# Kernel tuning notes

Measured on AMD Instinct MI355X. Metric: run time of the kernel, lower is better.

The kernel has to match this reference:

```python
import jax, jax.numpy as jnp
import numpy as np
from jax import lax

SCORE_THRESHOLD = 0.001
IOU_THRESHOLD = 0.7
MAX_DETECTIONS = 300
PRE_NMS_TOPK = 1024      # standard pre-NMS candidate cap (torchvision/YOLO practice)
CLASS_OFFSET = 4096.0    # > max image coord, separates classes so cross-class IoU == 0
IMG = 640.0

B, N, C = 32, 8400, 80


def setup_inputs() -> dict:
    key = jax.random.key(0)
    kc, ks, kp = jax.random.split(key, 3)
    # well-formed boxes in [y1, x1, y2, x2] convention (matches repo's nms())
    tl = jax.random.uniform(kc, (B, N, 2), jnp.float32, 0.0, IMG - 1.0)   # (y1, x1)
    wh = jax.random.uniform(ks, (B, N, 2), jnp.float32, 4.0, 160.0)      # (h, w)
    boxes = jnp.concatenate([tl, jnp.minimum(tl + wh, IMG)], axis=-1)     # [B,N,4]
    scores = jax.random.uniform(kp, (B, N, C), jnp.float32)               # [B,N,C]
    return {"boxes": boxes, "scores": scores}


def _pairwise_iou(b):
    # b: [B,K,4] as [y1,x1,y2,x2]; +1 pixel convention per the repo's nms()
    y1, x1, y2, x2 = b[..., 0], b[..., 1], b[..., 2], b[..., 3]
    areas = (x2 - x1 + 1.0) * (y2 - y1 + 1.0)                             # [B,K]
    yy1 = jnp.maximum(y1[:, :, None], y1[:, None, :])
    xx1 = jnp.maximum(x1[:, :, None], x1[:, None, :])
    yy2 = jnp.minimum(y2[:, :, None], y2[:, None, :])
    xx2 = jnp.minimum(x2[:, :, None], x2[:, None, :])
    w = jnp.maximum(0.0, xx2 - xx1 + 1.0)
    h = jnp.maximum(0.0, yy2 - yy1 + 1.0)
    inter = w * h                                                          # [B,K,K]
    return inter / (areas[:, :, None] + areas[:, None, :] - inter)


def multiclass_nms(boxes, scores):
    b, n, c = scores.shape
    flat = jnp.where(scores > SCORE_THRESHOLD, scores, 0.0).reshape(b, n * c)
    top_scores, top_idx = lax.top_k(flat, PRE_NMS_TOPK)                    # [B,K]
    box_idx = top_idx // c
    cls_idx = top_idx % c                                                  # int32 [B,K]
    cand = jnp.take_along_axis(boxes, box_idx[..., None], axis=1)          # [B,K,4]
    # offset boxes by class so per-class NMS happens in one shared pass
    off = cand + (cls_idx.astype(cand.dtype) * CLASS_OFFSET)[..., None]
    iou = _pairwise_iou(off)                                               # [B,K,K]

    k = PRE_NMS_TOPK
    idx = jnp.arange(k)
    keep0 = top_scores > SCORE_THRESHOLD                                   # [B,K]

    def body(i, keep):
        row = iou[:, i, :]                                                 # [B,K]
        sup = (row > IOU_THRESHOLD) & keep[:, i][:, None] & (idx[None, :] > i)
        return keep & ~sup

    keep = lax.fori_loop(0, k, body, keep0)                                # greedy NMS

    final_scores = jnp.where(keep, top_scores, 0.0)
    out_scores, sel = lax.top_k(final_scores, MAX_DETECTIONS)              # [B,300]
    out_boxes = jnp.take_along_axis(cand, sel[..., None], axis=1)          # [B,300,4]
    out_labels = jnp.take_along_axis(cls_idx, sel, axis=1)                 # [B,300]
    n_valid = jnp.minimum(jnp.sum(keep, axis=1, keepdims=True), MAX_DETECTIONS)
    return out_boxes, out_scores, out_labels.astype(jnp.int32), n_valid.astype(jnp.int32)


def reference(boxes, scores):
    return multiclass_nms(boxes, scores)
```

## Files before the change

### kernel.cpp

```cpp
#include <hip/hip_runtime.h>
#include <cstdint>
#include <cstddef>

#define B_      32
#define N_      8400
#define C_      80
#define NC      672000
#define NCV4    168000
#define NBINS   4096
#define TOPK    1024
#define MAXDET  300
#define CANDCAP 4096
#define NSLICE  16
#define SLICE_V4 10500
#define NBKT    8
#define SEGB    64
#define BSORT   256

#define STAGE_THRESH 0.998046875f

#define WS_SEGKEYS  0
#define WS_SEGCNT   2097152
#define WS_TOPSCORE 2113536
#define WS_TOPBOX   2244608
#define WS_TOPCLS   2768896
#define WS_KEEP     2899968

#define OUT_SCORES  38400
#define OUT_LABELS  48000
#define OUT_NVALID  57600

__global__ __launch_bounds__(256) void stage_kernel(const float4* __restrict__ scores4,
                                                    unsigned* __restrict__ segCnt,
                                                    unsigned long long* __restrict__ segKeys) {
    __shared__ unsigned lcnt[NBKT];
    int b = blockIdx.x, sl = blockIdx.y, tid = threadIdx.x;
    if (tid < NBKT) lcnt[tid] = 0;
    __syncthreads();
    const float4* s = scores4 + (size_t)b * NCV4 + (size_t)sl * SLICE_V4;
    for (int i = tid; i < SLICE_V4; i += 256) {
        float4 v = s[i];
        float c[4] = {v.x, v.y, v.z, v.w};
        unsigned flat0 = ((unsigned)sl * SLICE_V4 + (unsigned)i) * 4u;
        #pragma unroll
        for (int kc = 0; kc < 4; ++kc) {
            float x = (c[kc] > 0.001f) ? c[kc] : 0.0f;
            if (x >= STAGE_THRESH) {
                int bin = (int)(x * 4096.0f);
                bin = bin > (NBINS - 1) ? (NBINS - 1) : bin;
                int bkt = bin - 4088;
                unsigned p = atomicAdd(&lcnt[bkt], 1u);
                if (p < (unsigned)SEGB)
                    segKeys[(((size_t)(b * NBKT + bkt)) * NSLICE + sl) * SEGB + p] =
                        ((unsigned long long)__float_as_uint(x) << 32) |
                        (unsigned long long)(0xFFFFFFFFu - (flat0 + kc));
            }
        }
    }
    __syncthreads();
    if (tid < NBKT) segCnt[(b * NBKT + tid) * NSLICE + sl] = lcnt[tid];
}

__global__ __launch_bounds__(64) void sortb_kernel(
        const float4* __restrict__ scores4,
        const unsigned long long* __restrict__ segKeys,
        const unsigned* __restrict__ segCnt,
        const float4* __restrict__ boxes4,
        float* __restrict__ topScore,
        float4* __restrict__ topBox4,
        int* __restrict__ topCls) {
    __shared__ unsigned long long kbuf[CANDCAP];
    __shared__ unsigned bsum[NBKT];
    __shared__ unsigned bok[NBKT];
    __shared__ unsigned spref[NSLICE + 1];
    __shared__ unsigned scnt;
    __shared__ int s_cut;
    int b = blockIdx.x, bkt = blockIdx.y, lane = threadIdx.x;

    if (lane < NBKT) {
        const unsigned* c = segCnt + (b * NBKT + lane) * NSLICE;
        unsigned ssum = 0, ok = 1;
        for (int sl = 0; sl < NSLICE; ++sl) {
            unsigned v = c[sl];
            if (v > (unsigned)SEGB) ok = 0;
            ssum += v;
        }
        bsum[lane] = ssum; bok[lane] = ok;
    }
    __threadfence_block();
    unsigned M = 0, base = 0; int valid = 1;
    #pragma unroll
    for (int t = 0; t < NBKT; ++t) {
        unsigned s2 = bsum[t];
        if (!bok[t] || s2 > (unsigned)BSORT) valid = 0;
        M += s2;
        if (t > bkt) base += s2;
    }
    unsigned n = bsum[bkt];
    if (M < (unsigned)TOPK || M > (unsigned)CANDCAP) valid = 0;

    if (valid) {
        if (base >= (unsigned)TOPK || n == 0) return;
        if (lane == 0) {
            unsigned acc = 0; spref[0] = 0;
            const unsigned* c = segCnt + (b * NBKT + bkt) * NSLICE;
            for (int sl = 0; sl < NSLICE; ++sl) { acc += c[sl]; spref[sl + 1] = acc; }
        }
        __threadfence_block();
        for (int sl = 0; sl < NSLICE; ++sl) {
            unsigned b0 = spref[sl], c2 = spref[sl + 1] - b0;
            const unsigned long long* src =
                segKeys + (((size_t)(b * NBKT + bkt)) * NSLICE + sl) * SEGB;
            for (unsigned t = lane; t < c2; t += 64) kbuf[b0 + t] = src[t];
        }
        for (unsigned t = n + lane; t < (unsigned)BSORT; t += 64) kbuf[t] = 0ull;
        __threadfence_block();
        for (int kk = 2; kk <= BSORT; kk <<= 1) {
            for (int j = kk >> 1; j > 0; j >>= 1) {
                for (int c2 = lane; c2 < BSORT / 2; c2 += 64) {
                    int t = ((c2 & ~(j - 1)) << 1) | (c2 & (j - 1));
                    int l = t | j;
                    unsigned long long a0 = kbuf[t], c0 = kbuf[l];
                    bool sw = ((t & kk) == 0) ? (a0 < c0) : (a0 > c0);
                    if (sw) { kbuf[t] = c0; kbuf[l] = a0; }
                }
                __threadfence_block();
            }
        }
        unsigned wlim = (unsigned)TOPK - base; if (wlim > n) wlim = n;
        for (unsigned r = lane; r < wlim; r += 64) {
            unsigned long long key = kbuf[r];
            float sc = __uint_as_float((unsigned)(key >> 32));
            unsigned idx = 0xFFFFFFFFu - (unsigned)(key & 0xFFFFFFFFull);
            if (idx >= (unsigned)NC) idx = 0;
            unsigned bi = idx / (unsigned)C_;
            unsigned cl = idx - bi * (unsigned)C_;
            unsigned pos = base + r;
            topScore[b * TOPK + pos] = sc;
            topBox4[b * TOPK + pos] = boxes4[(size_t)b * N_ + bi];
            topCls[b * TOPK + pos] = (int)cl;
        }
        return;
    }

    if (bkt != 0) return;
    unsigned* fh = (unsigned*)kbuf;
    for (int i2 = lane; i2 < NBINS; i2 += 64) fh[i2] = 0;
    if (lane == 0) scnt = 0;
    __threadfence_block();
    const float4* s = scores4 + (size_t)b * NCV4;
    for (int i2 = lane; i2 < NCV4; i2 += 64) {
        float4 v = s[i2];
        float c4[4] = {v.x, v.y, v.z, v.w};
        #pragma unroll
        for (int kc = 0; kc < 4; ++kc) {
            float x = (c4[kc] > 0.001f) ? c4[kc] : 0.0f;
            int bin = (int)(x * 4096.0f);
            bin = bin > (NBINS - 1) ? (NBINS - 1) : bin;
            atomicAdd(&fh[bin], 1u);
        }
    }
    __threadfence_block();
    if (lane == 0) {
        unsigned acc = 0; int cb = 0;
        for (int bin = NBINS - 1; bin >= 0; --bin) {
            acc += fh[bin];
            if (acc >= (unsigned)TOPK) { cb = bin; break; }
        }
        s_cut = cb;
    }
    __threadfence_block();
    int cb = s_cut;
    for (int i2 = lane; i2 < NCV4; i2 += 64) {
        float4 v = s[i2];
        float c4[4] = {v.x, v.y, v.z, v.w};
        unsigned flat0 = (unsigned)i2 * 4u;
        #pragma unroll
        for (int kc = 0; kc < 4; ++kc) {
            float x = (c4[kc] > 0.001f) ? c4[kc] : 0.0f;
            int bin = (int)(x * 4096.0f);
            bin = bin > (NBINS - 1) ? (NBINS - 1) : bin;
            if (bin >= cb) {
                unsigned p = atomicAdd(&scnt, 1u);
                if (p < (unsigned)CANDCAP)
                    kbuf[p] = ((unsigned long long)__float_as_uint(x) << 32) |
                              (unsigned long long)(0xFFFFFFFFu - (flat0 + kc));
            }
        }
    }
    __threadfence_block();
    unsigned M2 = scnt; if (M2 > (unsigned)CANDCAP) M2 = CANDCAP;
    int S = (M2 <= 1024u) ? 1024 : (M2 <= 2048u ? 2048 : CANDCAP);
    for (int i2 = (int)M2 + lane; i2 < S; i2 += 64) kbuf[i2] = 0ull;
    __threadfence_block();
    for (int kk = 2; kk <= S; kk <<= 1) {
        for (int j = kk >> 1; j > 0; j >>= 1) {
            for (int t = lane; t < S; t += 64) {
                int l = t ^ j;
                if (l > t) {
                    unsigned long long a0 = kbuf[t], c0 = kbuf[l];
                    bool sw = ((t & kk) == 0) ? (a0 < c0) : (a0 > c0);
                    if (sw) { kbuf[t] = c0; kbuf[l] = a0; }
                }
            }
            __threadfence_block();
        }
    }
    for (int r = lane; r < TOPK; r += 64) {
        unsigned long long key = kbuf[r];
        float sc = __uint_as_float((unsigned)(key >> 32));
        unsigned idx = 0xFFFFFFFFu - (unsigned)(key & 0xFFFFFFFFull);
        if (idx >= (unsigned)NC) idx = 0;
        unsigned bi = idx / (unsigned)C_;
        unsigned cl = idx - bi * (unsigned)C_;
        topScore[b * TOPK + r] = sc;
        topBox4[b * TOPK + r] = boxes4[(size_t)b * N_ + bi];
        topCls[b * TOPK + r] = (int)cl;
    }
}

#define CLS_CAP 256
__global__ __launch_bounds__(64) void nms_kernel(const float* __restrict__ topScore,
                                                 const float* __restrict__ topBox,
                                                 const int* __restrict__ topCls,
                                                 int* __restrict__ keep) {
    __shared__ unsigned short pos[CLS_CAP];
    __shared__ float by1[CLS_CAP], bx1[CLS_CAP], by2[CLS_CAP], bx2[CLS_CAP];
    __shared__ float barea[CLS_CAP];
    __shared__ unsigned char sup[CLS_CAP];
    int b = blockIdx.x;
    int c = blockIdx.y;
    int lane = threadIdx.x;
    const float* ts = topScore + b * TOPK;
    const int*   tc = topCls + b * TOPK;
    int*         kp = keep + b * TOPK;
    float off = (float)c * 4096.0f;
    int base = 0;
    for (int chunkS = 0; chunkS < TOPK; chunkS += 64) {
        int i = chunkS + lane;
        int cls = tc[i];
        float sc = ts[i];
        bool mine = (cls == c);
        bool listed = mine && (sc > 0.001f);
        if (mine) kp[i] = 0;
        unsigned long long mask = __ballot(listed);
        int rank = __popcll(mask & ((1ull << lane) - 1ull));
        if (listed) {
            int slot = base + rank;
            if (slot < CLS_CAP) {
                pos[slot] = (unsigned short)i;
                const float* tb = topBox + ((size_t)(b * TOPK + i)) * 4;
                float y1 = tb[0] + off, x1 = tb[1] + off;
                float y2 = tb[2] + off, x2 = tb[3] + off;
                by1[slot] = y1; bx1[slot] = x1; by2[slot] = y2; bx2[slot] = x2;
                barea[slot] = __fmul_rn((x2 - x1) + 1.0f, (y2 - y1) + 1.0f);
                sup[slot] = 0;
            }
        }
        base += __popcll(mask);
    }
    int m = base < CLS_CAP ? base : CLS_CAP;
    __syncthreads();
    int cur = 0;
    while (cur < m) {
        if (lane == 0) kp[pos[cur]] = 1;
        float cy1 = by1[cur], cx1 = bx1[cur], cy2 = by2[cur], cx2 = bx2[cur];
        float carea = barea[cur];
        for (int j = cur + 1 + lane; j < m; j += 64) {
            if (!sup[j]) {
                float yy1 = fmaxf(cy1, by1[j]), xx1 = fmaxf(cx1, bx1[j]);
                float yy2 = fminf(cy2, by2[j]), xx2 = fminf(cx2, bx2[j]);
                float w = fmaxf(0.0f, (xx2 - xx1) + 1.0f);
                float h = fmaxf(0.0f, (yy2 - yy1) + 1.0f);
                float inter = __fmul_rn(w, h);
                float denom = (carea + barea[j]) - inter;
                float iou = inter / denom;
                if (iou > 0.7f) sup[j] = 1;
            }
        }
        __syncthreads();
        int nxt = m;
        for (int j = cur + 1 + lane; j < m; j += 64)
            if (!sup[j]) { nxt = j; break; }
        for (int o = 32; o > 0; o >>= 1) {
            int other = __shfl_xor(nxt, o, 64);
            nxt = nxt < other ? nxt : other;
        }
        cur = nxt;
    }
}

__global__ __launch_bounds__(1024) void finalize_kernel(const float* __restrict__ topScore,
                                                        const float* __restrict__ topBox,
                                                        const int* __restrict__ topCls,
                                                        const int* __restrict__ keep,
                                                        float* __restrict__ out) {
    __shared__ int sk[TOPK];
    __shared__ int sel[MAXDET];
    int b = blockIdx.x;
    int i = threadIdx.x;
    int kp = keep[b * TOPK + i];
    sk[i] = kp;
    __syncthreads();
    for (int off = 1; off < TOPK; off <<= 1) {
        int add = (i >= off) ? sk[i - off] : 0;
        __syncthreads();
        sk[i] += add;
        __syncthreads();
    }
    int nk = sk[TOPK - 1];
    int incl = sk[i];
    int kexcl = incl - kp;
    int sexcl = i - kexcl;
    if (kp) {
        if (kexcl < MAXDET) sel[kexcl] = i;
    } else {
        int slot = nk + sexcl;
        if (slot < MAXDET) sel[slot] = i;
    }
    __syncthreads();
    if (i < MAXDET) {
        int p = sel[i];
        float sc = (i < nk) ? topScore[b * TOPK + p] : 0.0f;
        const float* tb = topBox + ((size_t)b * TOPK + p) * 4;
        float* ob = out + ((size_t)b * MAXDET + i) * 4;
        ob[0] = tb[0]; ob[1] = tb[1]; ob[2] = tb[2]; ob[3] = tb[3];
        out[OUT_SCORES + b * MAXDET + i] = sc;
        out[OUT_LABELS + b * MAXDET + i] = (float)topCls[b * TOPK + p];
    }
    if (i == 0) out[OUT_NVALID + b] = (float)(nk < MAXDET ? nk : MAXDET);
}

extern "C" void kernel_launch(void* const* d_in, const int* in_sizes, int n_in,
                              void* d_out, int out_size, void* d_ws, size_t ws_size,
                              hipStream_t stream) {
    const float* boxes  = (const float*)d_in[0];
    const float* scores = (const float*)d_in[1];
    float* out = (float*)d_out;
    char* ws = (char*)d_ws;

    unsigned long long* segKeys = (unsigned long long*)(ws + WS_SEGKEYS);
    unsigned* segCnt = (unsigned*)(ws + WS_SEGCNT);
    float* topScore = (float*)(ws + WS_TOPSCORE);
    float* topBox = (float*)(ws + WS_TOPBOX);
    int* topCls = (int*)(ws + WS_TOPCLS);
    int* keep = (int*)(ws + WS_KEEP);

    const float4* scores4 = (const float4*)scores;
    const float4* boxes4  = (const float4*)boxes;

    stage_kernel<<<dim3(B_, NSLICE), 256, 0, stream>>>(scores4, segCnt, segKeys);
    sortb_kernel<<<dim3(B_, NBKT), 64, 0, stream>>>(scores4, segKeys, segCnt, boxes4,
                                                    topScore, (float4*)topBox, topCls);
    nms_kernel<<<dim3(B_, C_), 64, 0, stream>>>(topScore, topBox, topCls, keep);
    finalize_kernel<<<B_, 1024, 0, stream>>>(topScore, topBox, topCls, keep, out);
}
```

Before: 190.0 us.

## Fuse sort, per-class NMS and finalize into one per-image block kernel

Replaces the sort, NMS and finalize kernels with a single 1024-thread block per image that keeps top-K scores, classes, boxes and keep flags in shared memory. The bitonic sort of each bucket becomes a rank-by-counting sort, and per-class NMS runs as 16 waves each handling several classes with the per-class cap lowered to 128. This removes two kernel launches and the global-memory round trips for intermediates. In exchange each image now runs on only 32 blocks, so NMS parallelism across classes drops from 80 blocks per image to 16 waves, and the fallback path runs within one block per image.

New measurement: 223.5 us. 1.18x slower.

```diff
diff --git a/kernel.cpp b/kernel.cpp
--- a/kernel.cpp
+++ b/kernel.cpp
@@ -16,15 +16,12 @@
 #define NBKT    8
 #define SEGB    64
 #define BSORT   256
+#define CLS_CAP 128
 
 #define STAGE_THRESH 0.998046875f
 
 #define WS_SEGKEYS  0
 #define WS_SEGCNT   2097152
-#define WS_TOPSCORE 2113536
-#define WS_TOPBOX   2244608
-#define WS_TOPCLS   2768896
-#define WS_KEEP     2899968
 
 #define OUT_SCORES  38400
 #define OUT_LABELS  48000
@@ -61,274 +58,287 @@
     if (tid < NBKT) segCnt[(b * NBKT + tid) * NSLICE + sl] = lcnt[tid];
 }
 
-__global__ __launch_bounds__(64) void sortb_kernel(
+__global__ __launch_bounds__(1024) void fused_kernel(
         const float4* __restrict__ scores4,
         const unsigned long long* __restrict__ segKeys,
         const unsigned* __restrict__ segCnt,
         const float4* __restrict__ boxes4,
-        float* __restrict__ topScore,
-        float4* __restrict__ topBox4,
-        int* __restrict__ topCls) {
-    __shared__ unsigned long long kbuf[CANDCAP];
+        float* __restrict__ out) {
+    __shared__ unsigned scnt2[NBKT][NSLICE];
     __shared__ unsigned bsum[NBKT];
     __shared__ unsigned bok[NBKT];
-    __shared__ unsigned spref[NSLICE + 1];
-    __shared__ unsigned scnt;
-    __shared__ int s_cut;
-    int b = blockIdx.x, bkt = blockIdx.y, lane = threadIdx.x;
-
-    if (lane < NBKT) {
-        const unsigned* c = segCnt + (b * NBKT + lane) * NSLICE;
+    __shared__ unsigned spref[NBKT][NSLICE];
+    __shared__ float   sScore[TOPK];
+    __shared__ int     sCls[TOPK];
+    __shared__ int     sBoxIdx[TOPK];
+    __shared__ float4  sBox[TOPK];
+    __shared__ int     sKeep[TOPK];
+    __shared__ int     sk[TOPK];
+    __shared__ int     sel[MAXDET];
+    __shared__ int     s_cut;
+    __shared__ unsigned s_scnt;
+    __shared__ __align__(16) char upool[49152];
+    unsigned long long* kbuf = (unsigned long long*)upool;
+    unsigned* fh = (unsigned*)(upool + 32768);
+    float* ny1 = (float*)upool;
+    float* nx1 = ny1 + 16 * CLS_CAP;
+    float* ny2 = nx1 + 16 * CLS_CAP;
+    float* nx2 = ny2 + 16 * CLS_CAP;
+    float* nar = nx2 + 16 * CLS_CAP;
+    unsigned short* npos = (unsigned short*)(nar + 16 * CLS_CAP);
+    unsigned char*  nsup = (unsigned char*)(npos + 16 * CLS_CAP);
+
+    int b = blockIdx.x;
+    int tid = threadIdx.x;
+    int lane = tid & 63;
+    int wave = tid >> 6;
+
+    if (tid < NBKT * NSLICE)
+        scnt2[tid >> 4][tid & 15] = segCnt[b * NBKT * NSLICE + tid];
+    __syncthreads();
+    if (tid < NBKT) {
         unsigned ssum = 0, ok = 1;
+        #pragma unroll
         for (int sl = 0; sl < NSLICE; ++sl) {
-            unsigned v = c[sl];
+            unsigned v = scnt2[tid][sl];
             if (v > (unsigned)SEGB) ok = 0;
             ssum += v;
         }
-        bsum[lane] = ssum; bok[lane] = ok;
-    }
-    __threadfence_block();
-    unsigned M = 0, base = 0; int valid = 1;
+        bsum[tid] = ssum; bok[tid] = ok;
+    }
+    if (tid < NBKT * NSLICE) {
+        int bkt = tid >> 4, sl = tid & 15;
+        unsigned acc = 0;
+        for (int s2 = 0; s2 < sl; ++s2) acc += scnt2[bkt][s2];
+        spref[bkt][sl] = acc;
+    }
+    __syncthreads();
+    unsigned M = 0; int valid = 1;
     #pragma unroll
     for (int t = 0; t < NBKT; ++t) {
         unsigned s2 = bsum[t];
         if (!bok[t] || s2 > (unsigned)BSORT) valid = 0;
         M += s2;
-        if (t > bkt) base += s2;
-    }
-    unsigned n = bsum[bkt];
+    }
     if (M < (unsigned)TOPK || M > (unsigned)CANDCAP) valid = 0;
 
     if (valid) {
-        if (base >= (unsigned)TOPK || n == 0) return;
-        if (lane == 0) {
-            unsigned acc = 0; spref[0] = 0;
-            const unsigned* c = segCnt + (b * NBKT + bkt) * NSLICE;
-            for (int sl = 0; sl < NSLICE; ++sl) { acc += c[sl]; spref[sl + 1] = acc; }
-        }
-        __threadfence_block();
-        for (int sl = 0; sl < NSLICE; ++sl) {
-            unsigned b0 = spref[sl], c2 = spref[sl + 1] - b0;
+        for (int seg = wave; seg < NBKT * NSLICE; seg += 16) {
+            int bkt = seg >> 4, sl = seg & 15;
+            unsigned c2 = scnt2[bkt][sl];
             const unsigned long long* src =
                 segKeys + (((size_t)(b * NBKT + bkt)) * NSLICE + sl) * SEGB;
-            for (unsigned t = lane; t < c2; t += 64) kbuf[b0 + t] = src[t];
-        }
-        for (unsigned t = n + lane; t < (unsigned)BSORT; t += 64) kbuf[t] = 0ull;
-        __threadfence_block();
-        for (int kk = 2; kk <= BSORT; kk <<= 1) {
+            if ((unsigned)lane < c2)
+                kbuf[bkt * BSORT + spref[bkt][sl] + lane] = src[lane];
+        }
+        __syncthreads();
+        int bkt = tid >> 7;
+        unsigned n = bsum[bkt];
+        unsigned base = 0;
+        for (int t = bkt + 1; t < NBKT; ++t) base += bsum[t];
+        if (base < (unsigned)TOPK && n > 0) {
+            const unsigned long long* kb = kbuf + bkt * BSORT;
+            int j0 = tid & 127, j1 = j0 + 128;
+            unsigned long long k0 = (j0 < (int)n) ? kb[j0] : 0ull;
+            unsigned long long k1 = (j1 < (int)n) ? kb[j1] : 0ull;
+            unsigned r0 = 0, r1 = 0;
+            for (unsigned i = 0; i < n; ++i) {
+                unsigned long long ki = kb[i];
+                r0 += (ki > k0); r1 += (ki > k1);
+            }
+            if (j0 < (int)n) {
+                unsigned pos = base + r0;
+                if (pos < (unsigned)TOPK) {
+                    unsigned idx = 0xFFFFFFFFu - (unsigned)(k0 & 0xFFFFFFFFull);
+                    if (idx >= (unsigned)NC) idx = 0;
+                    unsigned bi = idx / (unsigned)C_;
+                    sScore[pos] = __uint_as_float((unsigned)(k0 >> 32));
+                    sCls[pos] = (int)(idx - bi * (unsigned)C_);
+                    sBoxIdx[pos] = (int)bi;
+                }
+            }
+            if (j1 < (int)n) {
+                unsigned pos = base + r1;
+                if (pos < (unsigned)TOPK) {
+                    unsigned idx = 0xFFFFFFFFu - (unsigned)(k1 & 0xFFFFFFFFull);
+                    if (idx >= (unsigned)NC) idx = 0;
+                    unsigned bi = idx / (unsigned)C_;
+                    sScore[pos] = __uint_as_float((unsigned)(k1 >> 32));
+                    sCls[pos] = (int)(idx - bi * (unsigned)C_);
+                    sBoxIdx[pos] = (int)bi;
+                }
+            }
+        }
+    } else {
+        for (int i = tid; i < NBINS; i += 1024) fh[i] = 0;
+        if (tid == 0) s_scnt = 0;
+        __syncthreads();
+        const float4* s = scores4 + (size_t)b * NCV4;
+        for (int i = tid; i < NCV4; i += 1024) {
+            float4 v = s[i];
+            float c4[4] = {v.x, v.y, v.z, v.w};
+            #pragma unroll
+            for (int kc = 0; kc < 4; ++kc) {
+                float x = (c4[kc] > 0.001f) ? c4[kc] : 0.0f;
+                int bin = (int)(x * 4096.0f);
+                bin = bin > (NBINS - 1) ? (NBINS - 1) : bin;
+                atomicAdd(&fh[bin], 1u);
+            }
+        }
+        __syncthreads();
+        if (tid == 0) {
+            unsigned acc = 0; int cb2 = 0;
+            for (int bin = NBINS - 1; bin >= 0; --bin) {
+                acc += fh[bin];
+                if (acc >= (unsigned)TOPK) { cb2 = bin; break; }
+            }
+            s_cut = cb2;
+        }
+        __syncthreads();
+        int cb = s_cut;
+        for (int i = tid; i < NCV4; i += 1024) {
+            float4 v = s[i];
+            float c4[4] = {v.x, v.y, v.z, v.w};
+            unsigned flat0 = (unsigned)i * 4u;
+            #pragma unroll
+            for (int kc = 0; kc < 4; ++kc) {
+                float x = (c4[kc] > 0.001f) ? c4[kc] : 0.0f;
+                int bin = (int)(x * 4096.0f);
+                bin = bin > (NBINS - 1) ? (NBINS - 1) : bin;
+                if (bin >= cb) {
+                    unsigned p = atomicAdd(&s_scnt, 1u);
+                    if (p < (unsigned)CANDCAP)
+                        kbuf[p] = ((unsigned long long)__float_as_uint(x) << 32) |
+                                  (unsigned long long)(0xFFFFFFFFu - (flat0 + kc));
+                }
+            }
+        }
+        __syncthreads();
+        unsigned M2 = s_scnt; if (M2 > (unsigned)CANDCAP) M2 = CANDCAP;
+        int S = (M2 <= 1024u) ? 1024 : (M2 <= 2048u ? 2048 : CANDCAP);
+        for (int i = (int)M2 + tid; i < S; i += 1024) kbuf[i] = 0ull;
+        __syncthreads();
+        for (int kk = 2; kk <= S; kk <<= 1) {
             for (int j = kk >> 1; j > 0; j >>= 1) {
-                for (int c2 = lane; c2 < BSORT / 2; c2 += 64) {
-                    int t = ((c2 & ~(j - 1)) << 1) | (c2 & (j - 1));
-                    int l = t | j;
-                    unsigned long long a0 = kbuf[t], c0 = kbuf[l];
-                    bool sw = ((t & kk) == 0) ? (a0 < c0) : (a0 > c0);
-                    if (sw) { kbuf[t] = c0; kbuf[l] = a0; }
-                }
-                __threadfence_block();
-            }
-        }
-        unsigned wlim = (unsigned)TOPK - base; if (wlim > n) wlim = n;
-        for (unsigned r = lane; r < wlim; r += 64) {
+                for (int t = tid; t < S; t += 1024) {
+                    int l = t ^ j;
+                    if (l > t) {
+                        unsigned long long a0 = kbuf[t], c0 = kbuf[l];
+                        bool sw = ((t & kk) == 0) ? (a0 < c0) : (a0 > c0);
+                        if (sw) { kbuf[t] = c0; kbuf[l] = a0; }
+                    }
+                }
+                __syncthreads();
+            }
+        }
+        for (int r = tid; r < TOPK; r += 1024) {
             unsigned long long key = kbuf[r];
-            float sc = __uint_as_float((unsigned)(key >> 32));
             unsigned idx = 0xFFFFFFFFu - (unsigned)(key & 0xFFFFFFFFull);
             if (idx >= (unsigned)NC) idx = 0;
             unsigned bi = idx / (unsigned)C_;
-            unsigned cl = idx - bi * (unsigned)C_;
-            unsigned pos = base + r;
-            topScore[b * TOPK + pos] = sc;
-            topBox4[b * TOPK + pos] = boxes4[(size_t)b * N_ + bi];
-            topCls[b * TOPK + pos] = (int)cl;
-        }
-        return;
-    }
-
-    if (bkt != 0) return;
-    unsigned* fh = (unsigned*)kbuf;
-    for (int i2 = lane; i2 < NBINS; i2 += 64) fh[i2] = 0;
-    if (lane == 0) scnt = 0;
-    __threadfence_block();
-    const float4* s = scores4 + (size_t)b * NCV4;
-    for (int i2 = lane; i2 < NCV4; i2 += 64) {
-        float4 v = s[i2];
-        float c4[4] = {v.x, v.y, v.z, v.w};
-        #pragma unroll
-        for (int kc = 0; kc < 4; ++kc) {
-            float x = (c4[kc] > 0.001f) ? c4[kc] : 0.0f;
-            int bin = (int)(x * 4096.0f);
-            bin = bin > (NBINS - 1) ? (NBINS - 1) : bin;
-            atomicAdd(&fh[bin], 1u);
-        }
-    }
-    __threadfence_block();
-    if (lane == 0) {
-        unsigned acc = 0; int cb = 0;
-        for (int bin = NBINS - 1; bin >= 0; --bin) {
-            acc += fh[bin];
-            if (acc >= (unsigned)TOPK) { cb = bin; break; }
-        }
-        s_cut = cb;
-    }
-    __threadfence_block();
-    int cb = s_cut;
-    for (int i2 = lane; i2 < NCV4; i2 += 64) {
-        float4 v = s[i2];
-        float c4[4] = {v.x, v.y, v.z, v.w};
-        unsigned flat0 = (unsigned)i2 * 4u;
-        #pragma unroll
-        for (int kc = 0; kc < 4; ++kc) {
-            float x = (c4[kc] > 0.001f) ? c4[kc] : 0.0f;
-            int bin = (int)(x * 4096.0f);
-            bin = bin > (NBINS - 1) ? (NBINS - 1) : bin;
-            if (bin >= cb) {
-                unsigned p = atomicAdd(&scnt, 1u);
-                if (p < (unsigned)CANDCAP)
-                    kbuf[p] = ((unsigned long long)__float_as_uint(x) << 32) |
-                              (unsigned long long)(0xFFFFFFFFu - (flat0 + kc));
-            }
-        }
-    }
-    __threadfence_block();
-    unsigned M2 = scnt; if (M2 > (unsigned)CANDCAP) M2 = CANDCAP;
-    int S = (M2 <= 1024u) ? 1024 : (M2 <= 2048u ? 2048 : CANDCAP);
-    for (int i2 = (int)M2 + lane; i2 < S; i2 += 64) kbuf[i2] = 0ull;
-    __threadfence_block();
-    for (int kk = 2; kk <= S; kk <<= 1) {
-        for (int j = kk >> 1; j > 0; j >>= 1) {
-            for (int t = lane; t < S; t += 64) {
-                int l = t ^ j;
-                if (l > t) {
-                    unsigned long long a0 = kbuf[t], c0 = kbuf[l];
-                    bool sw = ((t & kk) == 0) ? (a0 < c0) : (a0 > c0);
-                    if (sw) { kbuf[t] = c0; kbuf[l] = a0; }
+            sScore[r] = __uint_as_float((unsigned)(key >> 32));
+            sCls[r] = (int)(idx - bi * (unsigned)C_);
+            sBoxIdx[r] = (int)bi;
+        }
+    }
+    __syncthreads();
+
+    {
+        int bi = sBoxIdx[tid];
+        sKeep[tid] = 0;
+        sBox[tid] = boxes4[(size_t)b * N_ + bi];
+    }
+    __syncthreads();
+
+    for (int c = wave; c < C_; c += 16) {
+        float off = (float)c * 4096.0f;
+        int base2 = 0;
+        for (int chunkS = 0; chunkS < TOPK; chunkS += 64) {
+            int i = chunkS + lane;
+            int cls = sCls[i];
+            float sc = sScore[i];
+            bool listed = (cls == c) && (sc > 0.001f);
+            unsigned long long mask = __ballot(listed);
+            int rank = __popcll(mask & ((1ull << lane) - 1ull));
+            if (listed) {
+                int slot = base2 + rank;
+                if (slot < CLS_CAP) {
+                    int s5 = wave * CLS_CAP + slot;
+                    float4 tb = sBox[i];
+                    float y1 = tb.x + off, x1 = tb.y + off;
+                    float y2 = tb.z + off, x2 = tb.w + off;
+                    npos[s5] = (unsigned short)i;
+                    ny1[s5] = y1; nx1[s5] = x1; ny2[s5] = y2; nx2[s5] = x2;
+                    nar[s5] = __fmul_rn((x2 - x1) + 1.0f, (y2 - y1) + 1.0f);
+                    nsup[s5] = 0;
+                }
+            }
+            base2 += __popcll(mask);
+        }
+        int m = base2 < CLS_CAP ? base2 : CLS_CAP;
+        __threadfence_block();
+        int cur = 0;
+        while (cur < m) {
+            int sc5 = wave * CLS_CAP + cur;
+            if (lane == 0) sKeep[npos[sc5]] = 1;
+            float cy1 = ny1[sc5], cx1 = nx1[sc5], cy2 = ny2[sc5], cx2 = nx2[sc5];
+            float carea = nar[sc5];
+            for (int j = cur + 1 + lane; j < m; j += 64) {
+                int t5 = wave * CLS_CAP + j;
+                if (!nsup[t5]) {
+                    float yy1 = fmaxf(cy1, ny1[t5]), xx1 = fmaxf(cx1, nx1[t5]);
+                    float yy2 = fminf(cy2, ny2[t5]), xx2 = fminf(cx2, nx2[t5]);
+                    float w = fmaxf(0.0f, (xx2 - xx1) + 1.0f);
+                    float h = fmaxf(0.0f, (yy2 - yy1) + 1.0f);
+                    float inter = __fmul_rn(w, h);
+                    float denom = (carea + nar[t5]) - inter;
+                    float iou = inter / denom;
+                    if (iou > 0.7f) nsup[t5] = 1;
                 }
             }
             __threadfence_block();
-        }
-    }
-    for (int r = lane; r < TOPK; r += 64) {
-        unsigned long long key = kbuf[r];
-        float sc = __uint_as_float((unsigned)(key >> 32));
-        unsigned idx = 0xFFFFFFFFu - (unsigned)(key & 0xFFFFFFFFull);
-        if (idx >= (unsigned)NC) idx = 0;
-        unsigned bi = idx / (unsigned)C_;
-        unsigned cl = idx - bi * (unsigned)C_;
-        topScore[b * TOPK + r] = sc;
-        topBox4[b * TOPK + r] = boxes4[(size_t)b * N_ + bi];
-        topCls[b * TOPK + r] = (int)cl;
-    }
-}
-
-#define CLS_CAP 256
-__global__ __launch_bounds__(64) void nms_kernel(const float* __restrict__ topScore,
-                                                 const float* __restrict__ topBox,
-                                                 const int* __restrict__ topCls,
-                                                 int* __restrict__ keep) {
-    __shared__ unsigned short pos[CLS_CAP];
-    __shared__ float by1[CLS_CAP], bx1[CLS_CAP], by2[CLS_CAP], bx2[CLS_CAP];
-    __shared__ float barea[CLS_CAP];
-    __shared__ unsigned char sup[CLS_CAP];
-    int b = blockIdx.x;
-    int c = blockIdx.y;
-    int lane = threadIdx.x;
-    const float* ts = topScore + b * TOPK;
-    const int*   tc = topCls + b * TOPK;
-    int*         kp = keep + b * TOPK;
-    float off = (float)c * 4096.0f;
-    int base = 0;
-    for (int chunkS = 0; chunkS < TOPK; chunkS += 64) {
-        int i = chunkS + lane;
-        int cls = tc[i];
-        float sc = ts[i];
-        bool mine = (cls == c);
-        bool listed = mine && (sc > 0.001f);
-        if (mine) kp[i] = 0;
-        unsigned long long mask = __ballot(listed);
-        int rank = __popcll(mask & ((1ull << lane) - 1ull));
-        if (listed) {
-            int slot = base + rank;
-            if (slot < CLS_CAP) {
-                pos[slot] = (unsigned short)i;
-                const float* tb = topBox + ((size_t)(b * TOPK + i)) * 4;
-                float y1 = tb[0] + off, x1 = tb[1] + off;
-                float y2 = tb[2] + off, x2 = tb[3] + off;
-                by1[slot] = y1; bx1[slot] = x1; by2[slot] = y2; bx2[slot] = x2;
-                barea[slot] = __fmul_rn((x2 - x1) + 1.0f, (y2 - y1) + 1.0f);
-                sup[slot] = 0;
-            }
-        }
-        base += __popcll(mask);
-    }
-    int m = base < CLS_CAP ? base : CLS_CAP;
-    __syncthreads();
-    int cur = 0;
-    while (cur < m) {
-        if (lane == 0) kp[pos[cur]] = 1;
-        float cy1 = by1[cur], cx1 = bx1[cur], cy2 = by2[cur], cx2 = bx2[cur];
-        float carea = barea[cur];
-        for (int j = cur + 1 + lane; j < m; j += 64) {
-            if (!sup[j]) {
-                float yy1 = fmaxf(cy1, by1[j]), xx1 = fmaxf(cx1, bx1[j]);
-                float yy2 = fminf(cy2, by2[j]), xx2 = fminf(cx2, bx2[j]);
-                float w = fmaxf(0.0f, (xx2 - xx1) + 1.0f);
-                float h = fmaxf(0.0f, (yy2 - yy1) + 1.0f);
-                float inter = __fmul_rn(w, h);
-                float denom = (carea + barea[j]) - inter;
-                float iou = inter / denom;
-                if (iou > 0.7f) sup[j] = 1;
-            }
-        }
-        __syncthreads();
-        int nxt = m;
-        for (int j = cur + 1 + lane; j < m; j += 64)
-            if (!sup[j]) { nxt = j; break; }
-        for (int o = 32; o > 0; o >>= 1) {
-            int other = __shfl_xor(nxt, o, 64);
-            nxt = nxt < other ? nxt : other;
-        }
-        cur = nxt;
-    }
-}
-
-__global__ __launch_bounds__(1024) void finalize_kernel(const float* __restrict__ topScore,
-                                                        const float* __restrict__ topBox,
-                                                        const int* __restrict__ topCls,
-                                                        const int* __restrict__ keep,
-                                                        float* __restrict__ out) {
-    __shared__ int sk[TOPK];
-    __shared__ int sel[MAXDET];
-    int b = blockIdx.x;
-    int i = threadIdx.x;
-    int kp = keep[b * TOPK + i];
-    sk[i] = kp;
-    __syncthreads();
-    for (int off = 1; off < TOPK; off <<= 1) {
-        int add = (i >= off) ? sk[i - off] : 0;
-        __syncthreads();
-        sk[i] += add;
+            int nxt = m;
+            for (int j = cur + 1 + lane; j < m; j += 64)
+                if (!nsup[wave * CLS_CAP + j]) { nxt = j; break; }
+            for (int o = 32; o > 0; o >>= 1) {
+                int other = __shfl_xor(nxt, o, 64);
+                nxt = nxt < other ? nxt : other;
+            }
+            cur = nxt;
+        }
+    }
+    __syncthreads();
+
+    int kp = sKeep[tid];
+    sk[tid] = kp;
+    __syncthreads();
+    for (int off2 = 1; off2 < TOPK; off2 <<= 1) {
+        int add = (tid >= off2) ? sk[tid - off2] : 0;
+        __syncthreads();
+        sk[tid] += add;
         __syncthreads();
     }
     int nk = sk[TOPK - 1];
-    int incl = sk[i];
+    int incl = sk[tid];
     int kexcl = incl - kp;
-    int sexcl = i - kexcl;
+    int sexcl = tid - kexcl;
     if (kp) {
-        if (kexcl < MAXDET) sel[kexcl] = i;
+        if (kexcl < MAXDET) sel[kexcl] = tid;
     } else {
         int slot = nk + sexcl;
-        if (slot < MAXDET) sel[slot] = i;
-    }
-    __syncthreads();
-    if (i < MAXDET) {
-        int p = sel[i];
-        float sc = (i < nk) ? topScore[b * TOPK + p] : 0.0f;
-        const float* tb = topBox + ((size_t)b * TOPK + p) * 4;
-        float* ob = out + ((size_t)b * MAXDET + i) * 4;
-        ob[0] = tb[0]; ob[1] = tb[1]; ob[2] = tb[2]; ob[3] = tb[3];
-        out[OUT_SCORES + b * MAXDET + i] = sc;
-        out[OUT_LABELS + b * MAXDET + i] = (float)topCls[b * TOPK + p];
-    }
-    if (i == 0) out[OUT_NVALID + b] = (float)(nk < MAXDET ? nk : MAXDET);
+        if (slot < MAXDET) sel[slot] = tid;
+    }
+    __syncthreads();
+    if (tid < MAXDET) {
+        int p = sel[tid];
+        float sc = (tid < nk) ? sScore[p] : 0.0f;
+        float4 tb = sBox[p];
+        float* ob = out + ((size_t)b * MAXDET + tid) * 4;
+        ob[0] = tb.x; ob[1] = tb.y; ob[2] = tb.z; ob[3] = tb.w;
+        out[OUT_SCORES + b * MAXDET + tid] = sc;
+        out[OUT_LABELS + b * MAXDET + tid] = (float)sCls[p];
+    }
+    if (tid == 0) out[OUT_NVALID + b] = (float)(nk < MAXDET ? nk : MAXDET);
 }
 
 extern "C" void kernel_launch(void* const* d_in, const int* in_sizes, int n_in,
@@ -341,17 +351,10 @@
 
     unsigned long long* segKeys = (unsigned long long*)(ws + WS_SEGKEYS);
     unsigned* segCnt = (unsigned*)(ws + WS_SEGCNT);
-    float* topScore = (float*)(ws + WS_TOPSCORE);
-    float* topBox = (float*)(ws + WS_TOPBOX);
-    int* topCls = (int*)(ws + WS_TOPCLS);
-    int* keep = (int*)(ws + WS_KEEP);
 
     const float4* scores4 = (const float4*)scores;
     const float4* boxes4  = (const float4*)boxes;
 
     stage_kernel<<<dim3(B_, NSLICE), 256, 0, stream>>>(scores4, segCnt, segKeys);
-    sortb_kernel<<<dim3(B_, NBKT), 64, 0, stream>>>(scores4, segKeys, segCnt, boxes4,
-                                                    topScore, (float4*)topBox, topCls);
-    nms_kernel<<<dim3(B_, C_), 64, 0, stream>>>(topScore, topBox, topCls, keep);
-    finalize_kernel<<<B_, 1024, 0, stream>>>(topScore, topBox, topCls, keep, out);
+    fused_kernel<<<B_, 1024, 0, stream>>>(scores4, segKeys, segCnt, boxes4, out);
 }
```

## Replace per-bucket bitonic sort with rank-by-counting and ballot-based finalize scan

Applied to the files above, without the earlier changes.

Each bucket of up to 256 candidates is now ordered by computing every key's rank through all-pairs comparison, and each key is written straight to its output position. This replaces the bitonic sort and its many barrier-separated passes. Segment counts are loaded once into shared memory with all lanes, and segment copies run across lanes in parallel instead of one slice at a time. The finalize kernel swaps its log-step shared-memory prefix scan for wave ballots plus popcount, and reads boxes as float4. The all-pairs ranking costs O(n^2) comparisons per bucket, but n is small.

Result: faster. 179.7 us (-5.4%).

```diff
diff --git a/kernel.cpp b/kernel.cpp
--- a/kernel.cpp
+++ b/kernel.cpp
@@ -61,7 +61,7 @@
     if (tid < NBKT) segCnt[(b * NBKT + tid) * NSLICE + sl] = lcnt[tid];
 }
 
-__global__ __launch_bounds__(64) void sortb_kernel(
+__global__ __launch_bounds__(64) void select_kernel(
         const float4* __restrict__ scores4,
         const unsigned long long* __restrict__ segKeys,
         const unsigned* __restrict__ segCnt,
@@ -70,75 +70,86 @@
         float4* __restrict__ topBox4,
         int* __restrict__ topCls) {
     __shared__ unsigned long long kbuf[CANDCAP];
-    __shared__ unsigned bsum[NBKT];
-    __shared__ unsigned bok[NBKT];
-    __shared__ unsigned spref[NSLICE + 1];
+    __shared__ unsigned scnt2[NBKT * NSLICE];
+    __shared__ unsigned spref[NSLICE];
     __shared__ unsigned scnt;
     __shared__ int s_cut;
     int b = blockIdx.x, bkt = blockIdx.y, lane = threadIdx.x;
 
-    if (lane < NBKT) {
-        const unsigned* c = segCnt + (b * NBKT + lane) * NSLICE;
-        unsigned ssum = 0, ok = 1;
-        for (int sl = 0; sl < NSLICE; ++sl) {
-            unsigned v = c[sl];
-            if (v > (unsigned)SEGB) ok = 0;
-            ssum += v;
-        }
-        bsum[lane] = ssum; bok[lane] = ok;
-    }
-    __threadfence_block();
-    unsigned M = 0, base = 0; int valid = 1;
+    scnt2[lane]      = segCnt[b * NBKT * NSLICE + lane];
+    scnt2[lane + 64] = segCnt[b * NBKT * NSLICE + lane + 64];
+    __threadfence_block();
+    unsigned M = 0, base = 0, n = 0; int valid = 1;
     #pragma unroll
     for (int t = 0; t < NBKT; ++t) {
-        unsigned s2 = bsum[t];
-        if (!bok[t] || s2 > (unsigned)BSORT) valid = 0;
+        unsigned s2 = 0, mx = 0;
+        #pragma unroll
+        for (int sl = 0; sl < NSLICE; ++sl) {
+            unsigned v = scnt2[t * NSLICE + sl];
+            s2 += v; mx = v > mx ? v : mx;
+        }
+        if (mx > (unsigned)SEGB || s2 > (unsigned)BSORT) valid = 0;
         M += s2;
         if (t > bkt) base += s2;
-    }
-    unsigned n = bsum[bkt];
+        if (t == bkt) n = s2;
+    }
     if (M < (unsigned)TOPK || M > (unsigned)CANDCAP) valid = 0;
 
     if (valid) {
         if (base >= (unsigned)TOPK || n == 0) return;
-        if (lane == 0) {
-            unsigned acc = 0; spref[0] = 0;
-            const unsigned* c = segCnt + (b * NBKT + bkt) * NSLICE;
-            for (int sl = 0; sl < NSLICE; ++sl) { acc += c[sl]; spref[sl + 1] = acc; }
+        if (lane < NSLICE) {
+            unsigned acc = 0;
+            for (int s2 = 0; s2 < lane; ++s2) acc += scnt2[bkt * NSLICE + s2];
+            spref[lane] = acc;
         }
         __threadfence_block();
-        for (int sl = 0; sl < NSLICE; ++sl) {
-            unsigned b0 = spref[sl], c2 = spref[sl + 1] - b0;
+        {
+            int sl = lane & 15;
+            int eo = lane >> 4;
+            unsigned cA = scnt2[bkt * NSLICE + sl];
+            unsigned b0 = spref[sl];
             const unsigned long long* src =
                 segKeys + (((size_t)(b * NBKT + bkt)) * NSLICE + sl) * SEGB;
-            for (unsigned t = lane; t < c2; t += 64) kbuf[b0 + t] = src[t];
-        }
-        for (unsigned t = n + lane; t < (unsigned)BSORT; t += 64) kbuf[t] = 0ull;
+            for (int e = eo; e < (int)cA; e += 4) kbuf[b0 + e] = src[e];
+            if (lane < 4) kbuf[n + lane] = 0ull;
+        }
         __threadfence_block();
-        for (int kk = 2; kk <= BSORT; kk <<= 1) {
-            for (int j = kk >> 1; j > 0; j >>= 1) {
-                for (int c2 = lane; c2 < BSORT / 2; c2 += 64) {
-                    int t = ((c2 & ~(j - 1)) << 1) | (c2 & (j - 1));
-                    int l = t | j;
-                    unsigned long long a0 = kbuf[t], c0 = kbuf[l];
-                    bool sw = ((t & kk) == 0) ? (a0 < c0) : (a0 > c0);
-                    if (sw) { kbuf[t] = c0; kbuf[l] = a0; }
+        int j0 = lane, j1 = lane + 64, j2 = lane + 128, j3 = lane + 192;
+        unsigned long long k0 = (j0 < (int)n) ? kbuf[j0] : 0ull;
+        unsigned long long k1 = (j1 < (int)n) ? kbuf[j1] : 0ull;
+        unsigned long long k2 = (j2 < (int)n) ? kbuf[j2] : 0ull;
+        unsigned long long k3 = (j3 < (int)n) ? kbuf[j3] : 0ull;
+        unsigned r0 = 0, r1 = 0, r2 = 0, r3 = 0;
+        for (unsigned i = 0; i < n; i += 4) {
+            unsigned long long a = kbuf[i], b2 = kbuf[i + 1];
+            unsigned long long c2 = kbuf[i + 2], d2 = kbuf[i + 3];
+            r0 += (unsigned)(a > k0) + (unsigned)(b2 > k0) +
+                  (unsigned)(c2 > k0) + (unsigned)(d2 > k0);
+            r1 += (unsigned)(a > k1) + (unsigned)(b2 > k1) +
+                  (unsigned)(c2 > k1) + (unsigned)(d2 > k1);
+            r2 += (unsigned)(a > k2) + (unsigned)(b2 > k2) +
+                  (unsigned)(c2 > k2) + (unsigned)(d2 > k2);
+            r3 += (unsigned)(a > k3) + (unsigned)(b2 > k3) +
+                  (unsigned)(c2 > k3) + (unsigned)(d2 > k3);
+        }
+        #pragma unroll
+        for (int q = 0; q < 4; ++q) {
+            int j = q == 0 ? j0 : q == 1 ? j1 : q == 2 ? j2 : j3;
+            unsigned long long k = q == 0 ? k0 : q == 1 ? k1 : q == 2 ? k2 : k3;
+            unsigned r = q == 0 ? r0 : q == 1 ? r1 : q == 2 ? r2 : r3;
+            if (j < (int)n) {
+                unsigned pos = base + r;
+                if (pos < (unsigned)TOPK) {
+                    float sc = __uint_as_float((unsigned)(k >> 32));
+                    unsigned idx = 0xFFFFFFFFu - (unsigned)(k & 0xFFFFFFFFull);
+                    if (idx >= (unsigned)NC) idx = 0;
+                    unsigned bi = idx / (unsigned)C_;
+                    unsigned cl = idx - bi * (unsigned)C_;
+                    topScore[b * TOPK + pos] = sc;
+                    topBox4[b * TOPK + pos] = boxes4[(size_t)b * N_ + bi];
+                    topCls[b * TOPK + pos] = (int)cl;
                 }
-                __threadfence_block();
-            }
-        }
-        unsigned wlim = (unsigned)TOPK - base; if (wlim > n) wlim = n;
-        for (unsigned r = lane; r < wlim; r += 64) {
-            unsigned long long key = kbuf[r];
-            float sc = __uint_as_float((unsigned)(key >> 32));
-            unsigned idx = 0xFFFFFFFFu - (unsigned)(key & 0xFFFFFFFFull);
-            if (idx >= (unsigned)NC) idx = 0;
-            unsigned bi = idx / (unsigned)C_;
-            unsigned cl = idx - bi * (unsigned)C_;
-            unsigned pos = base + r;
-            topScore[b * TOPK + pos] = sc;
-            topBox4[b * TOPK + pos] = boxes4[(size_t)b * N_ + bi];
-            topCls[b * TOPK + pos] = (int)cl;
+            }
         }
         return;
     }
@@ -295,40 +306,43 @@
                                                         const int* __restrict__ topCls,
                                                         const int* __restrict__ keep,
                                                         float* __restrict__ out) {
-    __shared__ int sk[TOPK];
+    __shared__ int wsum[16];
     __shared__ int sel[MAXDET];
     int b = blockIdx.x;
-    int i = threadIdx.x;
-    int kp = keep[b * TOPK + i];
-    sk[i] = kp;
-    __syncthreads();
-    for (int off = 1; off < TOPK; off <<= 1) {
-        int add = (i >= off) ? sk[i - off] : 0;
-        __syncthreads();
-        sk[i] += add;
-        __syncthreads();
-    }
-    int nk = sk[TOPK - 1];
-    int incl = sk[i];
-    int kexcl = incl - kp;
-    int sexcl = i - kexcl;
+    int tid = threadIdx.x;
+    int lane = tid & 63;
+    int wave = tid >> 6;
+    int kp = keep[b * TOPK + tid];
+    unsigned long long m = __ballot(kp != 0);
+    int wpre = __popcll(m & ((1ull << lane) - 1ull));
+    if (lane == 0) wsum[wave] = __popcll(m);
+    __syncthreads();
+    int wbase = 0, nk = 0;
+    #pragma unroll
+    for (int t = 0; t < 16; ++t) {
+        int v = wsum[t];
+        if (t < wave) wbase += v;
+        nk += v;
+    }
+    int kexcl = wbase + wpre;
+    int sexcl = tid - kexcl;
     if (kp) {
-        if (kexcl < MAXDET) sel[kexcl] = i;
+        if (kexcl < MAXDET) sel[kexcl] = tid;
     } else {
         int slot = nk + sexcl;
-        if (slot < MAXDET) sel[slot] = i;
-    }
-    __syncthreads();
-    if (i < MAXDET) {
-        int p = sel[i];
-        float sc = (i < nk) ? topScore[b * TOPK + p] : 0.0f;
-        const float* tb = topBox + ((size_t)b * TOPK + p) * 4;
-        float* ob = out + ((size_t)b * MAXDET + i) * 4;
-        ob[0] = tb[0]; ob[1] = tb[1]; ob[2] = tb[2]; ob[3] = tb[3];
-        out[OUT_SCORES + b * MAXDET + i] = sc;
-        out[OUT_LABELS + b * MAXDET + i] = (float)topCls[b * TOPK + p];
-    }
-    if (i == 0) out[OUT_NVALID + b] = (float)(nk < MAXDET ? nk : MAXDET);
+        if (slot < MAXDET) sel[slot] = tid;
+    }
+    __syncthreads();
+    if (tid < MAXDET) {
+        int p = sel[tid];
+        float sc = (tid < nk) ? topScore[b * TOPK + p] : 0.0f;
+        const float4 tb = ((const float4*)topBox)[(size_t)b * TOPK + p];
+        float* ob = out + ((size_t)b * MAXDET + tid) * 4;
+        ob[0] = tb.x; ob[1] = tb.y; ob[2] = tb.z; ob[3] = tb.w;
+        out[OUT_SCORES + b * MAXDET + tid] = sc;
+        out[OUT_LABELS + b * MAXDET + tid] = (float)topCls[b * TOPK + p];
+    }
+    if (tid == 0) out[OUT_NVALID + b] = (float)(nk < MAXDET ? nk : MAXDET);
 }
 
 extern "C" void kernel_launch(void* const* d_in, const int* in_sizes, int n_in,
@@ -350,8 +364,8 @@
     const float4* boxes4  = (const float4*)boxes;
 
     stage_kernel<<<dim3(B_, NSLICE), 256, 0, stream>>>(scores4, segCnt, segKeys);
-    sortb_kernel<<<dim3(B_, NBKT), 64, 0, stream>>>(scores4, segKeys, segCnt, boxes4,
-                                                    topScore, (float4*)topBox, topCls);
+    select_kernel<<<dim3(B_, NBKT), 64, 0, stream>>>(scores4, segKeys, segCnt, boxes4,
+                                                     topScore, (float4*)topBox, topCls);
     nms_kernel<<<dim3(B_, C_), 64, 0, stream>>>(topScore, topBox, topCls, keep);
     finalize_kernel<<<B_, 1024, 0, stream>>>(topScore, topBox, topCls, keep, out);
 }
```
